# Optimization experiments

Measured on AMD Instinct MI355X. Metric: run time of the kernel, lower is better.

The kernel has to match this reference:

```python
import jax, jax.numpy as jnp
import numpy as np
from jax import lax

WIN = 9
PAD = WIN // 2
DIM = 3
WIN_VOL = WIN ** DIM  # 729
EPS_DENOM = 1e-05


def _box_sum(x):
    # x: (N, 1, D, H, W); all-ones WINxWINxWIN box filter, 'same' padding
    kernel = jnp.ones((1, 1, WIN, WIN, WIN), dtype=x.dtype)
    return lax.conv_general_dilated(
        x, kernel,
        window_strides=(1, 1, 1),
        padding=[(PAD, PAD)] * 3,
        dimension_numbers=("NCDHW", "OIDHW", "NCDHW"),
    )


def setup_inputs() -> dict:
    key = jax.random.key(0)
    k1, k2 = jax.random.split(key)
    shape = (2, 1, 160, 192, 160)
    I = jax.random.uniform(k1, shape, dtype=jnp.float32)
    J = jax.random.uniform(k2, shape, dtype=jnp.float32)
    return {"I": I, "J": J}


def reference(I, J):
    n = I.shape[0]
    # Fuse the five box-filter convs into one by stacking along the batch dim
    stacked = jnp.concatenate([I, J, I * I, J * J, I * J], axis=0)
    sums = _box_sum(stacked)
    I_sum, J_sum, I2_sum, J2_sum, IJ_sum = (
        sums[0 * n:1 * n], sums[1 * n:2 * n], sums[2 * n:3 * n],
        sums[3 * n:4 * n], sums[4 * n:5 * n],
    )
    wv = jnp.asarray(WIN_VOL, dtype=I.dtype)
    E_I = I_sum / wv
    E_J = J_sum / wv
    cross = IJ_sum - I_sum * E_J - J_sum * E_I + E_I * E_J * wv
    I_var = I2_sum - 2 * E_I * I_sum + E_I * E_I * wv
    J_var = J2_sum - 2 * E_J * J_sum + E_J * E_J * wv
    cc = cross * cross / (I_var * J_var + EPS_DENOM)
    return -jnp.mean(cc)
```

## Files before the change

kernel.cpp:

```cpp
#include <hip/hip_runtime.h>


namespace {
constexpr int Wd = 160, Hd = 192, Dd = 160, NB = 2;
constexpr long DSTRIDE = (long)Hd * Wd;
constexpr long VOLUME  = (long)Dd * DSTRIDE;
constexpr long TOTAL   = VOLUME * NB;
constexpr int BW = 32, BH = 16, BD = 28;
constexpr int EH = BH + 8;
constexpr int NWB = 5, NHB = 12, NDB = 6;
constexpr int NBLK = NB * NDB * NHB * NWB;
constexpr int NT = 512;
constexpr int CH  = EH * BW;
constexpr int HWC = BH * BW;
constexpr float INV_WV = 1.0f / 729.0f;
}

__device__ __forceinline__ void bar_lds() {
    asm volatile("s_waitcnt lgkmcnt(0)\n\ts_barrier" ::: "memory");
}

__device__ __forceinline__ float4 slide9(float v0, float v1, float v2, float v3,
                                         float v4, float v5, float v6, float v7,
                                         float v8, float v9, float v10, float v11) {
    float s8 = ((v0 + v1) + (v2 + v3)) + ((v4 + v5) + (v6 + v7)) + v8;
    float4 o;
    o.x = s8;
    o.y = o.x + (v9 - v0);
    o.z = o.y + (v10 - v1);
    o.w = o.z + (v11 - v2);
    return o;
}

__global__ __launch_bounds__(NT) void k_ncc(const float* __restrict__ I,
                                            const float* __restrict__ J,
                                            float* __restrict__ partial) {
    __shared__ float ws[5 * CH];
    __shared__ float hw[5 * HWC];
    __shared__ float red[NT];

    const int tid = threadIdx.x;
    int bx = blockIdx.x;
    const int wb = bx % NWB; bx /= NWB;
    const int hb = bx % NHB; bx /= NHB;
    const int db = bx % NDB; bx /= NDB;
    const int n  = bx;
    const int w0 = wb * BW, h0 = hb * BH, d0 = db * BD;
    const long nvol = (long)n * VOLUME;

    const int seg = tid & 7;
    const int yy  = tid >> 3;
    const bool aJob = (tid < 192);
    const int ah    = h0 - 4 + yy;
    const int wbase = w0 - 4 + (seg << 2);
    const bool ahOk = aJob && ((unsigned)ah < (unsigned)Hd);
    const bool qok0 = ((unsigned)(wbase + 0) < (unsigned)Wd);
    const bool qok1 = ((unsigned)(wbase + 4) < (unsigned)Wd);
    const bool qok2 = ((unsigned)(wbase + 8) < (unsigned)Wd);
    const long roff = nvol + (long)ah * Wd + wbase + (long)(d0 - 4) * DSTRIDE;
    const float* aI = I + roff;
    const float* aJ = J + roff;

    const int c2  = tid >> 6;
    const int ho0 = ((tid >> 5) & 1) * 8;
    const int w2  = tid & 31;

    const int tx = tid & 31, ty = tid >> 5;

    float4 pI0, pI1, pI2, pJ0, pJ1, pJ2;

#define ISSUE(PP)                                                            \
    do {                                                                     \
        const bool _pv = ahOk && ((unsigned)(PP) < (unsigned)Dd);            \
        pI0 = (_pv && qok0) ? *(const float4*)(aI + 0) : float4{0, 0, 0, 0}; \
        pI1 = (_pv && qok1) ? *(const float4*)(aI + 4) : float4{0, 0, 0, 0}; \
        pI2 = (_pv && qok2) ? *(const float4*)(aI + 8) : float4{0, 0, 0, 0}; \
        pJ0 = (_pv && qok0) ? *(const float4*)(aJ + 0) : float4{0, 0, 0, 0}; \
        pJ1 = (_pv && qok1) ? *(const float4*)(aJ + 4) : float4{0, 0, 0, 0}; \
        pJ2 = (_pv && qok2) ? *(const float4*)(aJ + 8) : float4{0, 0, 0, 0}; \
    } while (0)

    float hist[9][5];
#pragma unroll
    for (int k = 0; k < 9; ++k)
#pragma unroll
        for (int c = 0; c < 5; ++c) hist[k][c] = 0.0f;
    float sa[5] = {0, 0, 0, 0, 0};
    float acc = 0.0f;

    ISSUE(d0 - 4);

#pragma unroll 1
    for (int M = 0; M < 4; ++M) {
#pragma unroll
        for (int u = 0; u < 9; ++u) {
            const int t = 9 * M + u;
            const int p = d0 - 4 + t;
            const bool pvalid = ((unsigned)p < (unsigned)Dd);

            if (pvalid && aJob) {
                const float a0 = pI0.x, a1 = pI0.y, a2 = pI0.z, a3 = pI0.w;
                const float a4 = pI1.x, a5 = pI1.y, a6 = pI1.z, a7 = pI1.w;
                const float a8 = pI2.x, a9 = pI2.y, a10 = pI2.z, a11 = pI2.w;
                const float b0 = pJ0.x, b1 = pJ0.y, b2 = pJ0.z, b3 = pJ0.w;
                const float b4 = pJ1.x, b5 = pJ1.y, b6 = pJ1.z, b7 = pJ1.w;
                const float b8 = pJ2.x, b9 = pJ2.y, b10 = pJ2.z, b11 = pJ2.w;
                float* const wab = ws + yy * BW + (seg << 2);
                *(float4*)(wab + 0 * CH) =
                    slide9(a0, a1, a2, a3, a4, a5, a6, a7, a8, a9, a10, a11);
                *(float4*)(wab + 1 * CH) =
                    slide9(b0, b1, b2, b3, b4, b5, b6, b7, b8, b9, b10, b11);
                *(float4*)(wab + 2 * CH) =
                    slide9(a0 * a0, a1 * a1, a2 * a2, a3 * a3, a4 * a4, a5 * a5,
                           a6 * a6, a7 * a7, a8 * a8, a9 * a9, a10 * a10, a11 * a11);
                *(float4*)(wab + 3 * CH) =
                    slide9(b0 * b0, b1 * b1, b2 * b2, b3 * b3, b4 * b4, b5 * b5,
                           b6 * b6, b7 * b7, b8 * b8, b9 * b9, b10 * b10, b11 * b11);
                *(float4*)(wab + 4 * CH) =
                    slide9(a0 * b0, a1 * b1, a2 * b2, a3 * b3, a4 * b4, a5 * b5,
                           a6 * b6, a7 * b7, a8 * b8, a9 * b9, a10 * b10, a11 * b11);
            }
            aI += DSTRIDE; aJ += DSTRIDE;
            ISSUE(p + 1);

            bar_lds();

            if (pvalid && tid < 320) {
                const float* const src = ws + c2 * CH + ho0 * BW + w2;
                float* const dst = hw + c2 * HWC + ho0 * BW + w2;
                float s = ((src[0 * BW] + src[1 * BW]) + (src[2 * BW] + src[3 * BW]))
                        + ((src[4 * BW] + src[5 * BW]) + (src[6 * BW] + src[7 * BW]));
#pragma unroll
                for (int k = 0; k < 8; ++k) {
                    s += src[(k + 8) * BW];
                    dst[k * BW] = s;
                    s -= src[k * BW];
                }
            }

            bar_lds();

            float h5[5];
            if (pvalid) {
#pragma unroll
                for (int c = 0; c < 5; ++c)
                    h5[c] = hw[c * HWC + ty * BW + tx];
            } else {
#pragma unroll
                for (int c = 0; c < 5; ++c) h5[c] = 0.0f;
            }
#pragma unroll
            for (int c = 0; c < 5; ++c) sa[c] += h5[c];
            const int dout = d0 + t - 8;
            if (t >= 8 && dout < Dd) {
                const float cross = sa[4] - sa[0] * sa[1] * INV_WV;
                const float iv    = sa[2] - sa[0] * sa[0] * INV_WV;
                const float jv    = sa[3] - sa[1] * sa[1] * INV_WV;
                acc += (cross * cross) * __builtin_amdgcn_rcpf(iv * jv + 1e-5f);
            }
#pragma unroll
            for (int c = 0; c < 5; ++c) sa[c] -= hist[(u + 1) % 9][c];
#pragma unroll
            for (int c = 0; c < 5; ++c) hist[u][c] = h5[c];
        }
    }
#undef ISSUE

    red[tid] = acc;
    __syncthreads();
    for (int off = NT / 2; off > 0; off >>= 1) {
        if (tid < off) red[tid] += red[tid + off];
        __syncthreads();
    }
    if (tid == 0) partial[blockIdx.x] = red[0];
}

__global__ __launch_bounds__(256) void k_final(const float* __restrict__ partial,
                                               float* __restrict__ out, int nparts) {
    __shared__ double red[256];
    double a = 0.0;
    for (int i = threadIdx.x; i < nparts; i += 256) a += (double)partial[i];
    red[threadIdx.x] = a;
    __syncthreads();
    for (int off = 128; off > 0; off >>= 1) {
        if (threadIdx.x < off) red[threadIdx.x] += red[threadIdx.x + off];
        __syncthreads();
    }
    if (threadIdx.x == 0) out[0] = (float)(-red[0] / (double)TOTAL);
}

extern "C" void kernel_launch(void* const* d_in, const int* in_sizes, int n_in,
                              void* d_out, int out_size, void* d_ws, size_t ws_size,
                              hipStream_t stream) {
    const float* I = (const float*)d_in[0];
    const float* J = (const float*)d_in[1];
    float* partial = (float*)d_ws;
    float* out = (float*)d_out;

    k_ncc<<<NBLK, NT, 0, stream>>>(I, J, partial);
    k_final<<<1, 256, 0, stream>>>(partial, out, NBLK);
}
```

Before: 161.5 us.

## Shrink depth tile, vectorize H-pass with float2, replace final kernel with atomics

Reduces the depth tile from 28 to 19 planes, raising the block count from 720 to 1080 for better occupancy and wave balance. The cost is a larger ratio of halo planes (8 per tile) to output planes. The vertical H-direction sliding sum now uses float2 LDS accesses handled by 160 threads instead of scalar accesses by 320. The second reduction kernel is replaced by a memset plus per-block float atomicAdd of scaled partials, which saves a launch but gives a nondeterministic float summation order.

```diff
diff --git a/kernel.cpp b/kernel.cpp
--- a/kernel.cpp
+++ b/kernel.cpp
@@ -5,15 +5,16 @@
 constexpr int Wd = 160, Hd = 192, Dd = 160, NB = 2;
 constexpr long DSTRIDE = (long)Hd * Wd;
 constexpr long VOLUME  = (long)Dd * DSTRIDE;
-constexpr long TOTAL   = VOLUME * NB;
-constexpr int BW = 32, BH = 16, BD = 28;
+constexpr int BW = 32, BH = 16, BD = 19;
 constexpr int EH = BH + 8;
-constexpr int NWB = 5, NHB = 12, NDB = 6;
+constexpr int NWB = 5, NHB = 12, NDB = 9;
 constexpr int NBLK = NB * NDB * NHB * NWB;
 constexpr int NT = 512;
 constexpr int CH  = EH * BW;
 constexpr int HWC = BH * BW;
+constexpr int NPLANES = BD + 8;
 constexpr float INV_WV = 1.0f / 729.0f;
+constexpr float NEG_INV_TOTAL = -1.0f / 9830400.0f;
 }
 
 __device__ __forceinline__ void bar_lds() {
@@ -34,7 +35,7 @@
 
 __global__ __launch_bounds__(NT) void k_ncc(const float* __restrict__ I,
                                             const float* __restrict__ J,
-                                            float* __restrict__ partial) {
+                                            float* __restrict__ out) {
     __shared__ float ws[5 * CH];
     __shared__ float hw[5 * HWC];
     __shared__ float red[NT];
@@ -61,9 +62,12 @@
     const float* aI = I + roff;
     const float* aJ = J + roff;
 
-    const int c2  = tid >> 6;
-    const int ho0 = ((tid >> 5) & 1) * 8;
-    const int w2  = tid & 31;
+    const int c2 = tid >> 5;
+    const int wp = tid & 15;
+    const int hq = (tid >> 4) & 1;
+    const float2* const a2srcB =
+        (const float2*)(ws + c2 * CH) + (hq * 8) * 16 + wp;
+    float2* const a2dstB = (float2*)(hw + c2 * HWC) + (hq * 8) * 16 + wp;
 
     const int tx = tid & 31, ty = tid >> 5;
 
@@ -91,7 +95,7 @@
     ISSUE(d0 - 4);
 
 #pragma unroll 1
-    for (int M = 0; M < 4; ++M) {
+    for (int M = 0; M < 3; ++M) {
 #pragma unroll
         for (int u = 0; u < 9; ++u) {
             const int t = 9 * M + u;
@@ -121,21 +125,32 @@
                            a6 * b6, a7 * b7, a8 * b8, a9 * b9, a10 * b10, a11 * b11);
             }
             aI += DSTRIDE; aJ += DSTRIDE;
-            ISSUE(p + 1);
+            if (t < NPLANES - 1) { ISSUE(p + 1); }
 
             bar_lds();
 
-            if (pvalid && tid < 320) {
-                const float* const src = ws + c2 * CH + ho0 * BW + w2;
-                float* const dst = hw + c2 * HWC + ho0 * BW + w2;
-                float s = ((src[0 * BW] + src[1 * BW]) + (src[2 * BW] + src[3 * BW]))
-                        + ((src[4 * BW] + src[5 * BW]) + (src[6 * BW] + src[7 * BW]));
-#pragma unroll
-                for (int k = 0; k < 8; ++k) {
-                    s += src[(k + 8) * BW];
-                    dst[k * BW] = s;
-                    s -= src[k * BW];
-                }
+            if (pvalid && tid < 160) {
+                const float2* const src = a2srcB;
+                float2* const dst = a2dstB;
+                const float2 g0 = src[0 * 16], g1 = src[1 * 16];
+                const float2 g2 = src[2 * 16], g3 = src[3 * 16];
+                const float2 g4 = src[4 * 16], g5 = src[5 * 16];
+                const float2 g6 = src[6 * 16], g7 = src[7 * 16];
+                float2 s;
+                s.x = ((g0.x + g1.x) + (g2.x + g3.x)) + ((g4.x + g5.x) + (g6.x + g7.x));
+                s.y = ((g0.y + g1.y) + (g2.y + g3.y)) + ((g4.y + g5.y) + (g6.y + g7.y));
+                float2 r;
+#define A2STEP(K, GK)                                                   \
+                r = src[(K + 8) * 16];                                  \
+                s.x += r.x; s.y += r.y;                                 \
+                dst[K * 16] = s;                                        \
+                s.x -= GK.x; s.y -= GK.y;
+                A2STEP(0, g0) A2STEP(1, g1) A2STEP(2, g2) A2STEP(3, g3)
+                A2STEP(4, g4) A2STEP(5, g5) A2STEP(6, g6)
+#undef A2STEP
+                r = src[15 * 16];
+                s.x += r.x; s.y += r.y;
+                dst[7 * 16] = s;
             }
 
             bar_lds();
@@ -172,21 +187,7 @@
         if (tid < off) red[tid] += red[tid + off];
         __syncthreads();
     }
-    if (tid == 0) partial[blockIdx.x] = red[0];
-}
-
-__global__ __launch_bounds__(256) void k_final(const float* __restrict__ partial,
-                                               float* __restrict__ out, int nparts) {
-    __shared__ double red[256];
-    double a = 0.0;
-    for (int i = threadIdx.x; i < nparts; i += 256) a += (double)partial[i];
-    red[threadIdx.x] = a;
-    __syncthreads();
-    for (int off = 128; off > 0; off >>= 1) {
-        if (threadIdx.x < off) red[threadIdx.x] += red[threadIdx.x + off];
-        __syncthreads();
-    }
-    if (threadIdx.x == 0) out[0] = (float)(-red[0] / (double)TOTAL);
+    if (tid == 0) atomicAdd(out, red[0] * NEG_INV_TOTAL);
 }
 
 extern "C" void kernel_launch(void* const* d_in, const int* in_sizes, int n_in,
@@ -194,9 +195,8 @@
                               hipStream_t stream) {
     const float* I = (const float*)d_in[0];
     const float* J = (const float*)d_in[1];
-    float* partial = (float*)d_ws;
     float* out = (float*)d_out;
 
-    k_ncc<<<NBLK, NT, 0, stream>>>(I, J, partial);
-    k_final<<<1, 256, 0, stream>>>(partial, out, NBLK);
-}
+    hipMemsetAsync(d_out, 0, sizeof(float), stream);
+    k_ncc<<<NBLK, NT, 0, stream>>>(I, J, out);
+}
```

Result: no change. 160.0 us (-0.9%).
